# Performance work log

Hardware: AMD Instinct MI355X
Metric: run time of the kernel (lower is better)

Reference implementation:

```python
import jax, jax.numpy as jnp
import numpy as np

EMB_DIM = 128
DEC_DIM = 128
NEG_INF = -1e10


def setup_inputs() -> dict:
    key = jax.random.key(0)
    k1, k2, k3, k4, k5, k6 = jax.random.split(key, 6)
    B, S = 64, 4096
    hidden = jax.random.normal(k1, (B, DEC_DIM), dtype=jnp.float32)
    seq_embs = jax.random.normal(k2, (S, B, EMB_DIM), dtype=jnp.float32)
    mask = jax.random.randint(k3, (B, S), 0, 2, dtype=jnp.int32)
    # nn.Linear(emb_dim + dec_dim, dec_dim): weight [dec_dim, emb_dim+dec_dim]
    fan_in = EMB_DIM + DEC_DIM
    bound = 1.0 / np.sqrt(fan_in)
    W_attn = jax.random.uniform(k4, (DEC_DIM, fan_in), minval=-bound, maxval=bound, dtype=jnp.float32)
    b_attn = jax.random.uniform(k5, (DEC_DIM,), minval=-bound, maxval=bound, dtype=jnp.float32)
    # nn.Linear(dec_dim, 1, bias=False): weight [1, dec_dim]
    bound_v = 1.0 / np.sqrt(DEC_DIM)
    v_w = jax.random.uniform(k6, (1, DEC_DIM), minval=-bound_v, maxval=bound_v, dtype=jnp.float32)
    return {"hidden": hidden, "seq_embs": seq_embs, "mask": mask,
            "W_attn": W_attn, "b_attn": b_attn, "v_w": v_w}


def reference(hidden, seq_embs, mask, W_attn, b_attn, v_w):
    # hidden: [B, Dd]; seq_embs: [S, B, De]; mask: [B, S]
    # Concat order in torch is (hidden, seq_embs) -> split W accordingly.
    Wh = W_attn[:, :DEC_DIM]   # [Dd, Dd] applied to hidden
    We = W_attn[:, DEC_DIM:]   # [Dd, De] applied to seq_embs
    embs = jnp.transpose(seq_embs, (1, 0, 2))            # [B, S, De]
    # energy = tanh(Linear(cat(hidden, embs))) without materializing concat
    h_proj = hidden @ Wh.T + b_attn                       # [B, Dd]
    e_proj = jnp.einsum('bse,de->bsd', embs, We)          # [B, S, Dd]
    energy = jnp.tanh(h_proj[:, None, :] + e_proj)        # [B, S, Dd]
    attention = jnp.einsum('bsd,d->bs', energy, v_w[0])   # [B, S]
    attention = jnp.where(mask == 0, NEG_INF, attention)
    return jax.nn.softmax(attention, axis=1)
```

## Files before the change

kernel.cpp:

```cpp
#include <hip/hip_runtime.h>
#include <hip/hip_bf16.h>

#define BB 64
#define SS 4096
#define EE 128
#define DD 128
#define FAN 256
#define NEG_INF_F (-1e10f)

typedef __bf16 bf16x8 __attribute__((ext_vector_type(8)));
typedef unsigned short u16x8 __attribute__((ext_vector_type(8)));
typedef float f32x4 __attribute__((ext_vector_type(4)));

__device__ inline bf16x8 ld_frag(const unsigned short* p) {
    union { u16x8 u; bf16x8 b; } c;
    c.u = *(const u16x8*)p;
    return c.b;
}

__device__ inline uint2 f4_to_bf4(float4 f) {
    union { __hip_bfloat162 b; unsigned u; } lo, hi;
    lo.b = __float22bfloat162_rn(make_float2(f.x, f.y));
    hi.b = __float22bfloat162_rn(make_float2(f.z, f.w));
    return make_uint2(lo.u, hi.u);
}

__device__ inline float tanh_fast(float x) {
    float ax = fabsf(x);
    float e = __expf(-2.0f * ax);
    float t = (1.0f - e) * __builtin_amdgcn_rcpf(1.0f + e);
    return x < 0.0f ? -t : t;
}

__global__ __launch_bounds__(256) void prep_kernel(
        const float* __restrict__ hidden, const float* __restrict__ W_attn,
        const float* __restrict__ b_attn, const float* __restrict__ v_w,
        float* __restrict__ hproj, unsigned short* __restrict__ Wb,
        float* __restrict__ v_out) {
    const int b = blockIdx.x;
    const int t = threadIdx.x;
    if (t < 128) {
        float acc = b_attn[t];
        const float* hrow = hidden + b * DD;
        const float* wrow = W_attn + t * FAN;
        #pragma unroll 8
        for (int e = 0; e < DD; e++) acc += hrow[e] * wrow[e];
        hproj[b * DD + t] = acc;
        if (b == 0) v_out[t] = v_w[t];
    } else {
        int tt = t - 128;
        int d  = 2 * b + (tt >> 6);
        int e0 = (tt & 63) * 2;
        float2 src = *(const float2*)(W_attn + d * FAN + DD + e0);
        union { __hip_bfloat162 bb; unsigned u; } c;
        c.bb = __float22bfloat162_rn(src);
        *(unsigned*)&Wb[d * EE + e0] = c.u;
    }
}

__global__ __launch_bounds__(256) void logits_kernel(
        const float* __restrict__ seq_embs, const int* __restrict__ mask,
        const float* __restrict__ hproj, const unsigned short* __restrict__ Wb,
        const float* __restrict__ v, float* __restrict__ logits) {
    __shared__ __attribute__((aligned(16))) unsigned short Ws[128][136];

    const int b    = blockIdx.y;
    const int s0   = blockIdx.x * 64;
    const int tid  = threadIdx.x;
    const int wave = tid >> 6;
    const int lane = tid & 63;
    const int m    = lane & 15;
    const int quad = lane >> 4;

    const int* __restrict__ mask_g = mask + (size_t)b * SS + s0;

    const uint4* __restrict__ Wb16 = (const uint4*)Wb;
    uint4 wstage[8];
    #pragma unroll
    for (int k = 0; k < 8; k++) wstage[k] = Wb16[tid + k * 256];

    const int arow = wave * 16 + m;
    const int am   = mask_g[arow];
    const float* xrow = seq_embs + (size_t)(s0 + arow) * (BB * EE)
                      + (size_t)b * EE + quad * 8;
    bf16x8 afrag[4];
    #pragma unroll
    for (int kk = 0; kk < 4; kk++) {
        union { uint4 q; bf16x8 bf; } c;
        c.q = make_uint4(0u, 0u, 0u, 0u);
        if (am != 0) {
            float4 f0 = *(const float4*)(xrow + kk * 32);
            float4 f1 = *(const float4*)(xrow + kk * 32 + 4);
            uint2 a = f4_to_bf4(f0), bq = f4_to_bf4(f1);
            c.q = make_uint4(a.x, a.y, bq.x, bq.y);
        }
        afrag[kk] = c.bf;
    }

    #pragma unroll
    for (int k = 0; k < 8; k++) {
        const int i = tid + k * 256;
        const int d = i >> 4, e8 = i & 15;
        *(uint4*)&Ws[d][e8 * 8] = wstage[k];
    }
    __syncthreads();

    f32x4 acc[8];
    #pragma unroll
    for (int t = 0; t < 8; t++) acc[t] = (f32x4){0.f, 0.f, 0.f, 0.f};
    #pragma unroll
    for (int kk = 0; kk < 4; kk++) {
        const int k0 = kk * 32 + quad * 8;
        #pragma unroll
        for (int t = 0; t < 8; t++) {
            bf16x8 bf = ld_frag(&Ws[t * 16 + m][k0]);
            acc[t] = __builtin_amdgcn_mfma_f32_16x16x32_bf16(afrag[kk], bf, acc[t], 0, 0, 0);
        }
    }

    float hp_r[8], v_r[8];
    #pragma unroll
    for (int t = 0; t < 8; t++) {
        hp_r[t] = hproj[b * DD + t * 16 + m];
        v_r[t]  = v[t * 16 + m];
    }
    const int4 mq = *(const int4*)(mask_g + wave * 16 + quad * 4);
    const int mqa[4] = {mq.x, mq.y, mq.z, mq.w};

    float red[4];
    #pragma unroll
    for (int r = 0; r < 4; r++) {
        float part = 0.f;
        if (mqa[r] != 0) {
            #pragma unroll
            for (int t = 0; t < 8; t++)
                part += v_r[t] * tanh_fast(hp_r[t] + acc[t][r]);
            part += __shfl_xor(part, 1);
            part += __shfl_xor(part, 2);
            part += __shfl_xor(part, 4);
            part += __shfl_xor(part, 8);
        }
        red[r] = (mqa[r] != 0) ? part : NEG_INF_F;
    }
    if (m == 0) {
        float4 o = make_float4(red[0], red[1], red[2], red[3]);
        *(float4*)&logits[(size_t)b * SS + s0 + wave * 16 + quad * 4] = o;
    }
}

__global__ __launch_bounds__(256) void softmax_kernel(float* __restrict__ logits) {
    const int b = blockIdx.x;
    const int tid = threadIdx.x;
    const int wave = tid >> 6;
    const int lane = tid & 63;
    float* row = logits + (size_t)b * SS;

    float4 vals[4];
    float lmax = -1e30f;
    #pragma unroll
    for (int i = 0; i < 4; i++) {
        vals[i] = *(const float4*)(row + (size_t)(i * 256 + tid) * 4);
        lmax = fmaxf(lmax, fmaxf(fmaxf(vals[i].x, vals[i].y), fmaxf(vals[i].z, vals[i].w)));
    }
    #pragma unroll
    for (int off = 32; off >= 1; off >>= 1)
        lmax = fmaxf(lmax, __shfl_xor(lmax, off));

    __shared__ float smax[4], ssum[4];
    if (lane == 0) smax[wave] = lmax;
    __syncthreads();
    const float gmax = fmaxf(fmaxf(smax[0], smax[1]), fmaxf(smax[2], smax[3]));

    float lsum = 0.f;
    #pragma unroll
    for (int i = 0; i < 4; i++) {
        vals[i].x = __expf(vals[i].x - gmax);
        vals[i].y = __expf(vals[i].y - gmax);
        vals[i].z = __expf(vals[i].z - gmax);
        vals[i].w = __expf(vals[i].w - gmax);
        lsum += (vals[i].x + vals[i].y) + (vals[i].z + vals[i].w);
    }
    #pragma unroll
    for (int off = 32; off >= 1; off >>= 1)
        lsum += __shfl_xor(lsum, off);
    if (lane == 0) ssum[wave] = lsum;
    __syncthreads();
    const float total = (ssum[0] + ssum[1]) + (ssum[2] + ssum[3]);
    const float inv = 1.0f / total;

    #pragma unroll
    for (int i = 0; i < 4; i++) {
        float4 o;
        o.x = vals[i].x * inv; o.y = vals[i].y * inv;
        o.z = vals[i].z * inv; o.w = vals[i].w * inv;
        *(float4*)(row + (size_t)(i * 256 + tid) * 4) = o;
    }
}

extern "C" void kernel_launch(void* const* d_in, const int* in_sizes, int n_in,
                              void* d_out, int out_size, void* d_ws, size_t ws_size,
                              hipStream_t stream) {
    const float* hidden   = (const float*)d_in[0];
    const float* seq_embs = (const float*)d_in[1];
    const int*   mask     = (const int*)d_in[2];
    const float* W_attn   = (const float*)d_in[3];
    const float* b_attn   = (const float*)d_in[4];
    const float* v_w      = (const float*)d_in[5];
    float* out = (float*)d_out;

    float*          hproj = (float*)d_ws;
    unsigned short* Wb    = (unsigned short*)((char*)d_ws + 32768);
    float*          vv    = (float*)((char*)d_ws + 65536);

    prep_kernel<<<64, 256, 0, stream>>>(hidden, W_attn, b_attn, v_w, hproj, Wb, vv);
    dim3 grid(SS / 64, BB);
    logits_kernel<<<grid, 256, 0, stream>>>(seq_embs, mask, hproj, Wb, vv, out);
    softmax_kernel<<<BB, 256, 0, stream>>>(out);
}
```

Measured before the change: 217.9 us.

## Process four sequence tiles per block with register double-buffered activation loads

Each logits block now handles four 64-row tiles instead of one. The W tile is staged into LDS once per block rather than once per 64 rows. The next tile's seq_embs rows are prefetched into a second register buffer while MFMA and tanh run on the current one, so global load latency can hide behind compute. It also sets a min-blocks-per-CU launch bound and vectorizes the hproj dot product in the prep kernel. The cost is a quarter as many blocks (1024) and higher register pressure, which could lower occupancy or cause spills.

```diff
diff --git a/kernel.cpp b/kernel.cpp
--- a/kernel.cpp
+++ b/kernel.cpp
@@ -6,6 +6,7 @@
 #define EE 128
 #define DD 128
 #define FAN 256
+#define TILES 4
 #define NEG_INF_F (-1e10f)
 
 typedef __bf16 bf16x8 __attribute__((ext_vector_type(8)));
@@ -41,10 +42,13 @@
     const int t = threadIdx.x;
     if (t < 128) {
         float acc = b_attn[t];
-        const float* hrow = hidden + b * DD;
-        const float* wrow = W_attn + t * FAN;
-        #pragma unroll 8
-        for (int e = 0; e < DD; e++) acc += hrow[e] * wrow[e];
+        const float4* hrow = (const float4*)(hidden + b * DD);
+        const float4* wrow = (const float4*)(W_attn + t * FAN);
+        #pragma unroll
+        for (int e = 0; e < 32; e++) {
+            float4 h = hrow[e], w = wrow[e];
+            acc += h.x * w.x + h.y * w.y + h.z * w.z + h.w * w.w;
+        }
         hproj[b * DD + t] = acc;
         if (b == 0) v_out[t] = v_w[t];
     } else {
@@ -58,65 +62,58 @@
     }
 }
 
-__global__ __launch_bounds__(256) void logits_kernel(
+__global__ __launch_bounds__(256, 4) void logits_kernel(
         const float* __restrict__ seq_embs, const int* __restrict__ mask,
         const float* __restrict__ hproj, const unsigned short* __restrict__ Wb,
         const float* __restrict__ v, float* __restrict__ logits) {
     __shared__ __attribute__((aligned(16))) unsigned short Ws[128][136];
 
     const int b    = blockIdx.y;
-    const int s0   = blockIdx.x * 64;
+    const int g    = blockIdx.x;
     const int tid  = threadIdx.x;
     const int wave = tid >> 6;
     const int lane = tid & 63;
     const int m    = lane & 15;
     const int quad = lane >> 4;
 
-    const int* __restrict__ mask_g = mask + (size_t)b * SS + s0;
+    const int arow = wave * 16 + m;
+
+    const int* __restrict__ mask_g = mask + (size_t)b * SS + g * (TILES * 64);
+    const float* __restrict__ xbase = seq_embs
+        + (size_t)(g * (TILES * 64) + arow) * (BB * EE)
+        + (size_t)b * EE + quad * 8;
 
     const uint4* __restrict__ Wb16 = (const uint4*)Wb;
     uint4 wstage[8];
     #pragma unroll
     for (int k = 0; k < 8; k++) wstage[k] = Wb16[tid + k * 256];
-
-    const int arow = wave * 16 + m;
-    const int am   = mask_g[arow];
-    const float* xrow = seq_embs + (size_t)(s0 + arow) * (BB * EE)
-                      + (size_t)b * EE + quad * 8;
-    bf16x8 afrag[4];
-    #pragma unroll
-    for (int kk = 0; kk < 4; kk++) {
-        union { uint4 q; bf16x8 bf; } c;
-        c.q = make_uint4(0u, 0u, 0u, 0u);
-        if (am != 0) {
-            float4 f0 = *(const float4*)(xrow + kk * 32);
-            float4 f1 = *(const float4*)(xrow + kk * 32 + 4);
-            uint2 a = f4_to_bf4(f0), bq = f4_to_bf4(f1);
-            c.q = make_uint4(a.x, a.y, bq.x, bq.y);
-        }
-        afrag[kk] = c.bf;
-    }
-
     #pragma unroll
     for (int k = 0; k < 8; k++) {
         const int i = tid + k * 256;
-        const int d = i >> 4, e8 = i & 15;
-        *(uint4*)&Ws[d][e8 * 8] = wstage[k];
+        *(uint4*)&Ws[i >> 4][(i & 15) * 8] = wstage[k];
+    }
+
+    int am[2];
+    int4 mq[2];
+    bf16x8 af[2][4];
+    {
+        am[0] = mask_g[arow];
+        mq[0] = *(const int4*)(mask_g + wave * 16 + quad * 4);
+        const float* xrow = xbase;
+        #pragma unroll
+        for (int kk = 0; kk < 4; kk++) {
+            union { uint4 q; bf16x8 bf; } c;
+            c.q = make_uint4(0u, 0u, 0u, 0u);
+            if (am[0] != 0) {
+                float4 f0 = *(const float4*)(xrow + kk * 32);
+                float4 f1 = *(const float4*)(xrow + kk * 32 + 4);
+                uint2 a = f4_to_bf4(f0), bq = f4_to_bf4(f1);
+                c.q = make_uint4(a.x, a.y, bq.x, bq.y);
+            }
+            af[0][kk] = c.bf;
+        }
     }
     __syncthreads();
-
-    f32x4 acc[8];
-    #pragma unroll
-    for (int t = 0; t < 8; t++) acc[t] = (f32x4){0.f, 0.f, 0.f, 0.f};
-    #pragma unroll
-    for (int kk = 0; kk < 4; kk++) {
-        const int k0 = kk * 32 + quad * 8;
-        #pragma unroll
-        for (int t = 0; t < 8; t++) {
-            bf16x8 bf = ld_frag(&Ws[t * 16 + m][k0]);
-            acc[t] = __builtin_amdgcn_mfma_f32_16x16x32_bf16(afrag[kk], bf, acc[t], 0, 0, 0);
-        }
-    }
 
     float hp_r[8], v_r[8];
     #pragma unroll
@@ -124,27 +121,63 @@
         hp_r[t] = hproj[b * DD + t * 16 + m];
         v_r[t]  = v[t * 16 + m];
     }
-    const int4 mq = *(const int4*)(mask_g + wave * 16 + quad * 4);
-    const int mqa[4] = {mq.x, mq.y, mq.z, mq.w};
-
-    float red[4];
-    #pragma unroll
-    for (int r = 0; r < 4; r++) {
-        float part = 0.f;
-        if (mqa[r] != 0) {
+
+    #pragma unroll
+    for (int tile = 0; tile < TILES; tile++) {
+        const int cur = tile & 1;
+        if (tile + 1 < TILES) {
+            const int nxt = cur ^ 1;
+            am[nxt] = mask_g[(tile + 1) * 64 + arow];
+            mq[nxt] = *(const int4*)(mask_g + (tile + 1) * 64 + wave * 16 + quad * 4);
+            const float* xrow = xbase + (size_t)((tile + 1) * 64) * (BB * EE);
             #pragma unroll
-            for (int t = 0; t < 8; t++)
-                part += v_r[t] * tanh_fast(hp_r[t] + acc[t][r]);
-            part += __shfl_xor(part, 1);
-            part += __shfl_xor(part, 2);
-            part += __shfl_xor(part, 4);
-            part += __shfl_xor(part, 8);
-        }
-        red[r] = (mqa[r] != 0) ? part : NEG_INF_F;
-    }
-    if (m == 0) {
-        float4 o = make_float4(red[0], red[1], red[2], red[3]);
-        *(float4*)&logits[(size_t)b * SS + s0 + wave * 16 + quad * 4] = o;
+            for (int kk = 0; kk < 4; kk++) {
+                union { uint4 q; bf16x8 bf; } c;
+                c.q = make_uint4(0u, 0u, 0u, 0u);
+                if (am[nxt] != 0) {
+                    float4 f0 = *(const float4*)(xrow + kk * 32);
+                    float4 f1 = *(const float4*)(xrow + kk * 32 + 4);
+                    uint2 a = f4_to_bf4(f0), bq = f4_to_bf4(f1);
+                    c.q = make_uint4(a.x, a.y, bq.x, bq.y);
+                }
+                af[nxt][kk] = c.bf;
+            }
+        }
+
+        f32x4 acc[8];
+        #pragma unroll
+        for (int t = 0; t < 8; t++) acc[t] = (f32x4){0.f, 0.f, 0.f, 0.f};
+        #pragma unroll
+        for (int kk = 0; kk < 4; kk++) {
+            const int k0 = kk * 32 + quad * 8;
+            #pragma unroll
+            for (int t = 0; t < 8; t++) {
+                bf16x8 bf = ld_frag(&Ws[t * 16 + m][k0]);
+                acc[t] = __builtin_amdgcn_mfma_f32_16x16x32_bf16(af[cur][kk], bf, acc[t], 0, 0, 0);
+            }
+        }
+
+        const int mqa[4] = {mq[cur].x, mq[cur].y, mq[cur].z, mq[cur].w};
+        float red[4];
+        #pragma unroll
+        for (int r = 0; r < 4; r++) {
+            float part = 0.f;
+            if (mqa[r] != 0) {
+                #pragma unroll
+                for (int t = 0; t < 8; t++)
+                    part += v_r[t] * tanh_fast(hp_r[t] + acc[t][r]);
+                part += __shfl_xor(part, 1);
+                part += __shfl_xor(part, 2);
+                part += __shfl_xor(part, 4);
+                part += __shfl_xor(part, 8);
+            }
+            red[r] = (mqa[r] != 0) ? part : NEG_INF_F;
+        }
+        if (m == 0) {
+            float4 o = make_float4(red[0], red[1], red[2], red[3]);
+            *(float4*)&logits[(size_t)b * SS + g * (TILES * 64) + tile * 64
+                              + wave * 16 + quad * 4] = o;
+        }
     }
 }
 
@@ -213,7 +246,7 @@
     float*          vv    = (float*)((char*)d_ws + 65536);
 
     prep_kernel<<<64, 256, 0, stream>>>(hidden, W_attn, b_attn, v_w, hproj, Wb, vv);
-    dim3 grid(SS / 64, BB);
+    dim3 grid(SS / (64 * TILES), BB);
     logits_kernel<<<grid, 256, 0, stream>>>(seq_embs, mask, hproj, Wb, vv, out);
     softmax_kernel<<<BB, 256, 0, stream>>>(out);
 }
```

After: 212.9 us, median of 2. -2.3%, faster.
